# Kernel tuning notes

Hardware: AMD Instinct MI355X
Metric: run time of the kernel (lower is better)

## Reference

```python
import jax, jax.numpy as jnp
import numpy as np

B, N, D, H, K = 8, 256, 128, 128, 8


def _kaiming_uniform(key, shape, fan_in):
    bound = np.sqrt(6.0 / fan_in)
    return jax.random.uniform(key, shape, jnp.float32, -bound, bound)


def setup_inputs() -> dict:
    key = jax.random.key(0)
    ks = jax.random.split(key, 5)
    E = jax.random.normal(ks[0], (B, N, D), jnp.float32)
    W1 = _kaiming_uniform(ks[1], (K, 2 * D, H), 2 * D)   # FFN2 layer 1
    b1 = jnp.zeros((K, H), jnp.float32)
    W2 = _kaiming_uniform(ks[2], (K, H, 2), H)           # FFN2 layer 2
    b2 = jnp.zeros((K, 2), jnp.float32)
    W3 = _kaiming_uniform(ks[3], (K, 2, 1), 2)           # FFN3
    b3 = jnp.zeros((K, 1), jnp.float32)
    return {"E": E, "W1": W1, "b1": b1, "W2": W2, "b2": b2, "W3": W3, "b3": b3}


def _entmax15_pair(logits):
    # Exact alpha=1.5 entmax over a last dim of size 2 (closed form).
    # z' = z/2; p_i = [z'_i - tau]_+^2 with sum(p)=1.
    t = (logits[..., 0] - logits[..., 1]) * 0.25   # signed half-gap of z'
    d = jnp.abs(t)
    s = jnp.sqrt(jnp.maximum(0.5 - d * d, 0.0))
    p0_interior = (s + t) ** 2                      # both coords in support
    p0 = jnp.where(d >= 0.5, (t > 0).astype(logits.dtype), p0_interior)
    return jnp.stack([p0, 1.0 - p0], axis=-1)


def reference(E, W1, b1, W2, b2, W3, b3):
    # E: [B,N,D]. Concat([Ei,Ej]) @ W1 == Ei @ W1[:D] + Ej @ W1[D:], so we never
    # materialize the [B,N,N,2D] pair tensor.
    Dd = E.shape[-1]
    W1i, W1j = W1[:, :Dd, :], W1[:, Dd:, :]
    outs = []
    for h in range(W1.shape[0]):  # small fixed head loop (k_basis)
        hi = jnp.einsum('bnd,dh->bnh', E, W1i[h])
        hj = jnp.einsum('bnd,dh->bnh', E, W1j[h])
        pre = hi[:, :, None, :] + hj[:, None, :, :] + b1[h]      # [B,N,N,H]
        act = jax.nn.relu(pre)                                    # dropout: eval mode (identity)
        logits2 = jnp.einsum('bijh,hc->bijc', act, W2[h]) + b2[h]  # [B,N,N,2]
        p2 = _entmax15_pair(logits2)
        a = jnp.einsum('bijc,co->bijo', p2, W3[h])[..., 0] + b3[h][0]  # [B,N,N]
        outs.append(a)
    M = jnp.stack(outs, axis=1)  # [B,K,N,N]
    n = E.shape[1]
    eye = jnp.eye(n, dtype=M.dtype)
    M = M * (1.0 - eye)[None, None]  # no_self_loop=True
    return M
```

## Files before the change

kernel.cpp:

```cpp
#include <hip/hip_runtime.h>
#include <hip/hip_fp16.h>
#include <cstdint>
#include <cstddef>

#define B_ 8
#define N_ 256
#define D_ 128
#define H_ 128
#define K_ 8

typedef _Float16 f16x8 __attribute__((ext_vector_type(8)));
typedef _Float16 f16x2 __attribute__((ext_vector_type(2)));
typedef float    f32x4 __attribute__((ext_vector_type(4)));

static __device__ __forceinline__ f16x2 h2cast(unsigned u) {
    return __builtin_bit_cast(f16x2, u);
}
static __device__ __forceinline__ unsigned packh2(float lo, float hi) {
    unsigned a = __half_as_ushort(__float2half(lo));
    unsigned b = __half_as_ushort(__float2half(hi));
    return a | (b << 16);
}

__global__ __launch_bounds__(256) void prep_all(
        const float* __restrict__ E, const float* __restrict__ W1,
        const float* __restrict__ W2, const float* __restrict__ b2,
        const float* __restrict__ W3, const float* __restrict__ b3,
        __half* __restrict__ Eh, __half* __restrict__ Wh,
        unsigned* __restrict__ wdh, float* __restrict__ consts) {
    __shared__ float Ws[128][33];
    const int bid = blockIdx.x;
    const int t   = threadIdx.x;

    if (bid < 256) {
        int idx = (bid * 256 + t) * 4;
        float4 v = *(const float4*)&E[idx];
        uint2 o;
        o.x = packh2(v.x, v.y);
        o.y = packh2(v.z, v.w);
        *(uint2*)&Eh[idx] = o;
    } else if (bid < 320) {
        const int kb = bid - 256;
        const int ct = kb & 7;
        const int k  = kb >> 3;
        const int c0 = ct * 32;
        const int ro = (c0 < 128) ? 0 : 128;
        const int h0 = c0 & 127;
        #pragma unroll
        for (int rep = 0; rep < 16; rep++) {
            int idx = rep * 256 + t;
            int d   = idx >> 5;
            int cl  = idx & 31;
            Ws[d][cl] = W1[((size_t)(k * 256 + ro + d)) * H_ + h0 + cl];
        }
        __syncthreads();
        const int cl = t >> 3;
        const int dg = t & 7;
        __half tmp[16];
        #pragma unroll
        for (int e = 0; e < 16; e++) tmp[e] = __float2half(Ws[dg * 16 + e][cl]);
        *(float4*)&Wh[((size_t)(k * 256 + c0 + cl)) * D_ + dg * 16]     = *(float4*)&tmp[0];
        *(float4*)&Wh[((size_t)(k * 256 + c0 + cl)) * D_ + dg * 16 + 8] = *(float4*)&tmp[8];
    } else {
        for (int idx = t; idx < K_ * 64; idx += 256) {
            int base = idx * 2;
            float w0 = W2[base * 2]     - W2[base * 2 + 1];
            float w1 = W2[base * 2 + 2] - W2[base * 2 + 3];
            wdh[idx] = packh2(w0, w1);
        }
        if (t < K_) {
            consts[t * 4 + 0] = b2[t * 2] - b2[t * 2 + 1];
            consts[t * 4 + 1] = W3[t * 2] - W3[t * 2 + 1];
            consts[t * 4 + 2] = W3[t * 2 + 1] + b3[t];
        }
    }
}

__global__ __launch_bounds__(256, 4) void fused_kernel(
        const __half* __restrict__ Eh, const __half* __restrict__ Wh,
        const float* __restrict__ b1, const unsigned* __restrict__ wdh,
        const float* __restrict__ consts, float* __restrict__ out) {
    __shared__ __half his[64 * 136];
    __shared__ __half hjs[64 * 136];

    const int bid = blockIdx.x;
    const int jt  = bid & 3;
    const int it  = (bid >> 2) & 3;
    const int bk  = bid >> 4;
    const int k   = bk & (K_ - 1);
    const int b   = bk >> 3;
    const int i0  = it * 64, j0 = jt * 64;
    const int t   = threadIdx.x;
    const int wv   = t >> 6;
    const int lane = t & 63;
    const int lr   = lane & 15, lk = lane >> 4;

    {
        const bool isJ   = (wv >= 2);
        const int  half32 = wv & 1;
        const int  rowbase = (isJ ? j0 : i0) + half32 * 32;
        const int  cbase   = isJ ? 128 : 0;
        __half* __restrict__ dst = isJ ? hjs : his;

        f16x8 A[2][4];
        #pragma unroll
        for (int mi = 0; mi < 2; mi++)
            #pragma unroll
            for (int kk = 0; kk < 4; kk++)
                A[mi][kk] = *(const f16x8*)&Eh[
                    ((size_t)(b * N_ + rowbase + mi * 16 + lr)) * D_ + kk * 32 + lk * 8];

        #pragma unroll
        for (int nc = 0; nc < 8; nc++) {
            f16x8 Bf[4];
            #pragma unroll
            for (int kk = 0; kk < 4; kk++)
                Bf[kk] = *(const f16x8*)&Wh[
                    ((size_t)(k * 256 + cbase + nc * 16 + lr)) * D_ + kk * 32 + lk * 8];
            const int hcol = nc * 16 + lr;
            const float bias = isJ ? 0.f : b1[k * H_ + hcol];
            #pragma unroll
            for (int mi = 0; mi < 2; mi++) {
                f32x4 acc = {0.f, 0.f, 0.f, 0.f};
                #pragma unroll
                for (int kk = 0; kk < 4; kk++)
                    acc = __builtin_amdgcn_mfma_f32_16x16x32_f16(A[mi][kk], Bf[kk], acc, 0, 0, 0);
                const int lrow = half32 * 32 + mi * 16 + lk * 4;
                #pragma unroll
                for (int q = 0; q < 4; q++)
                    dst[(lrow + q) * 136 + hcol] = __float2half(acc[q] + bias);
            }
        }
    }
    __syncthreads();

    const float b2d = consts[k * 4 + 0];
    const float w3d = consts[k * 4 + 1];
    const float w3b = consts[k * 4 + 2];
    const int tx = t & 15;
    const int ty = t >> 4;

    float acc[4][4];
    #pragma unroll
    for (int a = 0; a < 4; a++)
        #pragma unroll
        for (int c = 0; c < 4; c++) acc[a][c] = b2d;

    const unsigned* __restrict__ wp = wdh + k * 64;
    const f16x2 zz = {(_Float16)0, (_Float16)0};

    #pragma unroll 2
    for (int hq = 0; hq < 16; hq++) {
        unsigned Wv[4];
        *(uint4*)&Wv[0] = *(const uint4*)&wp[hq * 4];
        unsigned Aa[4][4], Bb[4][4];
        #pragma unroll
        for (int a = 0; a < 4; a++)
            *(uint4*)&Aa[a][0] = *(const uint4*)&his[(ty + 16 * a) * 136 + hq * 8];
        #pragma unroll
        for (int c = 0; c < 4; c++)
            *(uint4*)&Bb[c][0] = *(const uint4*)&hjs[(tx + 16 * c) * 136 + hq * 8];

        #pragma unroll
        for (int e = 0; e < 4; e++) {
            f16x2 w2 = h2cast(Wv[e]);
            #pragma unroll
            for (int a = 0; a < 4; a++) {
                f16x2 av = h2cast(Aa[a][e]);
                #pragma unroll
                for (int c = 0; c < 4; c++) {
                    f16x2 pre = av + h2cast(Bb[c][e]);
                    f16x2 act = __builtin_elementwise_max(pre, zz);
                    acc[a][c] = __builtin_amdgcn_fdot2(act, w2, acc[a][c], false);
                }
            }
        }
    }

    #pragma unroll
    for (int a = 0; a < 4; a++) {
        int i = i0 + ty + 16 * a;
        #pragma unroll
        for (int c = 0; c < 4; c++) {
            float av = acc[a][c];
            float tt = av * 0.25f;
            float dd = fabsf(tt);
            float ss = sqrtf(fmaxf(0.5f - dd * dd, 0.f));
            float p0i = (ss + tt) * (ss + tt);
            float p0 = (dd >= 0.5f) ? (tt > 0.f ? 1.f : 0.f) : p0i;
            float val = fmaf(p0, w3d, w3b);
            int j = j0 + tx + 16 * c;
            if (i == j) val = 0.f;
            out[((size_t)bk * N_ + i) * N_ + j] = val;
        }
    }
}

extern "C" void kernel_launch(void* const* d_in, const int* in_sizes, int n_in,
                              void* d_out, int out_size, void* d_ws, size_t ws_size,
                              hipStream_t stream) {
    (void)in_sizes; (void)n_in; (void)out_size; (void)ws_size;
    const float* E  = (const float*)d_in[0];
    const float* W1 = (const float*)d_in[1];
    const float* b1 = (const float*)d_in[2];
    const float* W2 = (const float*)d_in[3];
    const float* b2 = (const float*)d_in[4];
    const float* W3 = (const float*)d_in[5];
    const float* b3 = (const float*)d_in[6];
    float* out = (float*)d_out;

    char* ws = (char*)d_ws;
    unsigned* wdh    = (unsigned*)ws;
    float*    consts = (float*)(ws + 4096);
    __half*   Eh     = (__half*)(ws + 8192);
    __half*   Wh     = (__half*)(ws + 8192 + 524288);

    prep_all<<<321, 256, 0, stream>>>(E, W1, W2, b2, W3, b3, Eh, Wh, wdh, consts);
    fused_kernel<<<B_ * K_ * 16, 256, 0, stream>>>(Eh, Wh, b1, wdh, consts, out);
}
```

Measured before the change: 56.16 us.

## Enlarge pairwise tile to 128x64 and stage W2 diff weights in LDS

Each block now covers 128 i-rows by 64 j-columns, so every thread accumulates an 8x4 register tile instead of 4x4. This halves the block count and cuts the redundant per-block recomputation of the hj projection. The prologue GEMM is redistributed as three 16-row MFMA strips per wave, and the packed W2 differences are copied to shared memory instead of being read from global each iteration. The larger register tile lowers the launch-bounds occupancy target from 4 to 2 blocks, which risks less latency hiding and poorer load balance with 512 blocks.

```diff
diff --git a/kernel.cpp b/kernel.cpp
--- a/kernel.cpp
+++ b/kernel.cpp
@@ -76,39 +76,41 @@
     }
 }
 
-__global__ __launch_bounds__(256, 4) void fused_kernel(
+__global__ __launch_bounds__(256, 2) void fused_kernel(
         const __half* __restrict__ Eh, const __half* __restrict__ Wh,
         const float* __restrict__ b1, const unsigned* __restrict__ wdh,
         const float* __restrict__ consts, float* __restrict__ out) {
-    __shared__ __half his[64 * 136];
+    __shared__ __half his[128 * 136];
     __shared__ __half hjs[64 * 136];
+    __shared__ unsigned wlds[64];
 
     const int bid = blockIdx.x;
     const int jt  = bid & 3;
-    const int it  = (bid >> 2) & 3;
-    const int bk  = bid >> 4;
+    const int it  = (bid >> 2) & 1;
+    const int bk  = bid >> 3;
     const int k   = bk & (K_ - 1);
     const int b   = bk >> 3;
-    const int i0  = it * 64, j0 = jt * 64;
+    const int i0  = it * 128, j0 = jt * 64;
     const int t   = threadIdx.x;
     const int wv   = t >> 6;
     const int lane = t & 63;
     const int lr   = lane & 15, lk = lane >> 4;
 
-    {
-        const bool isJ   = (wv >= 2);
-        const int  half32 = wv & 1;
-        const int  rowbase = (isJ ? j0 : i0) + half32 * 32;
-        const int  cbase   = isJ ? 128 : 0;
-        __half* __restrict__ dst = isJ ? hjs : his;
-
-        f16x8 A[2][4];
-        #pragma unroll
-        for (int mi = 0; mi < 2; mi++)
-            #pragma unroll
-            for (int kk = 0; kk < 4; kk++)
-                A[mi][kk] = *(const f16x8*)&Eh[
-                    ((size_t)(b * N_ + rowbase + mi * 16 + lr)) * D_ + kk * 32 + lk * 8];
+    if (t < 64) wlds[t] = wdh[k * 64 + t];
+
+    #pragma unroll
+    for (int rb = 0; rb < 3; rb++) {
+        const int row16 = wv * 48 + rb * 16;
+        const bool isJ  = (row16 >= 128);
+        const int rowg  = isJ ? (j0 + row16 - 128) : (i0 + row16);
+        const int cbase = isJ ? 128 : 0;
+        __half* __restrict__ dst = isJ ? &hjs[(row16 - 128) * 136] : &his[row16 * 136];
+
+        f16x8 A[4];
+        #pragma unroll
+        for (int kk = 0; kk < 4; kk++)
+            A[kk] = *(const f16x8*)&Eh[
+                ((size_t)(b * N_ + rowg + lr)) * D_ + kk * 32 + lk * 8];
 
         #pragma unroll
         for (int nc = 0; nc < 8; nc++) {
@@ -119,17 +121,13 @@
                     ((size_t)(k * 256 + cbase + nc * 16 + lr)) * D_ + kk * 32 + lk * 8];
             const int hcol = nc * 16 + lr;
             const float bias = isJ ? 0.f : b1[k * H_ + hcol];
-            #pragma unroll
-            for (int mi = 0; mi < 2; mi++) {
-                f32x4 acc = {0.f, 0.f, 0.f, 0.f};
-                #pragma unroll
-                for (int kk = 0; kk < 4; kk++)
-                    acc = __builtin_amdgcn_mfma_f32_16x16x32_f16(A[mi][kk], Bf[kk], acc, 0, 0, 0);
-                const int lrow = half32 * 32 + mi * 16 + lk * 4;
-                #pragma unroll
-                for (int q = 0; q < 4; q++)
-                    dst[(lrow + q) * 136 + hcol] = __float2half(acc[q] + bias);
-            }
+            f32x4 acc = {0.f, 0.f, 0.f, 0.f};
+            #pragma unroll
+            for (int kk = 0; kk < 4; kk++)
+                acc = __builtin_amdgcn_mfma_f32_16x16x32_f16(A[kk], Bf[kk], acc, 0, 0, 0);
+            #pragma unroll
+            for (int q = 0; q < 4; q++)
+                dst[(lk * 4 + q) * 136 + hcol] = __float2half(acc[q] + bias);
         }
     }
     __syncthreads();
@@ -140,22 +138,21 @@
     const int tx = t & 15;
     const int ty = t >> 4;
 
-    float acc[4][4];
+    float acc[8][4];
     #pragma unroll
-    for (int a = 0; a < 4; a++)
+    for (int a = 0; a < 8; a++)
         #pragma unroll
         for (int c = 0; c < 4; c++) acc[a][c] = b2d;
 
-    const unsigned* __restrict__ wp = wdh + k * 64;
     const f16x2 zz = {(_Float16)0, (_Float16)0};
 
     #pragma unroll 2
     for (int hq = 0; hq < 16; hq++) {
         unsigned Wv[4];
-        *(uint4*)&Wv[0] = *(const uint4*)&wp[hq * 4];
-        unsigned Aa[4][4], Bb[4][4];
-        #pragma unroll
-        for (int a = 0; a < 4; a++)
+        *(uint4*)&Wv[0] = *(const uint4*)&wlds[hq * 4];
+        unsigned Aa[8][4], Bb[4][4];
+        #pragma unroll
+        for (int a = 0; a < 8; a++)
             *(uint4*)&Aa[a][0] = *(const uint4*)&his[(ty + 16 * a) * 136 + hq * 8];
         #pragma unroll
         for (int c = 0; c < 4; c++)
@@ -165,7 +162,7 @@
         for (int e = 0; e < 4; e++) {
             f16x2 w2 = h2cast(Wv[e]);
             #pragma unroll
-            for (int a = 0; a < 4; a++) {
+            for (int a = 0; a < 8; a++) {
                 f16x2 av = h2cast(Aa[a][e]);
                 #pragma unroll
                 for (int c = 0; c < 4; c++) {
@@ -178,7 +175,7 @@
     }
 
     #pragma unroll
-    for (int a = 0; a < 4; a++) {
+    for (int a = 0; a < 8; a++) {
         int i = i0 + ty + 16 * a;
         #pragma unroll
         for (int c = 0; c < 4; c++) {
@@ -216,5 +213,5 @@
     __half*   Wh     = (__half*)(ws + 8192 + 524288);
 
     prep_all<<<321, 256, 0, stream>>>(E, W1, W2, b2, W3, b3, Eh, Wh, wdh, consts);
-    fused_kernel<<<B_ * K_ * 16, 256, 0, stream>>>(Eh, Wh, b1, wdh, consts, out);
-}
+    fused_kernel<<<B_ * K_ * 8, 256, 0, stream>>>(Eh, Wh, b1, wdh, consts, out);
+}
```

Result: slower. 58.78 us (+4.7%).
